# Kernel tuning notes

Measured on AMD Instinct MI355X. Metric: run time of the kernel, lower is better.

Reference implementation:

```python
import jax, jax.numpy as jnp
import numpy as np

NUM_NODES = 10000
NUM_EDGES = 640000
D_FEAT = 128

def setup_inputs() -> dict:
    key = jax.random.key(0)
    k1, k2 = jax.random.split(key)
    x = jax.random.normal(k1, (NUM_NODES, D_FEAT), dtype=jnp.float32)
    edge_index = jax.random.randint(k2, (2, NUM_EDGES), 0, NUM_NODES, dtype=jnp.int64)
    return {"x": x, "edge_index": edge_index}

def reference(x, edge_index):
    # MessagePassing(aggr='add') with default message/update:
    # msg = x[src]; out[n] = sum of msg over edges with dst == n
    src, dst = edge_index[0], edge_index[1]
    msg = x[src]                                   # [num_edges, d]
    out = jax.ops.segment_sum(msg, dst, num_segments=NUM_NODES)  # [num_nodes, d]
    return out
```

## Files before the change

kernel.cpp:

```cpp
#include <hip/hip_runtime.h>

#define NUM_NODES 10000
#define NUM_EDGES 640000
#define D_FEAT 128

#define NPB 20
#define NB 500
#define K1_BLOCKS 256
#define EPB (NUM_EDGES / K1_BLOCKS)
#define CELL_CAP 16
#define INV 0xFFFFFFFFu
#define ZROW 10000u
#define STRIPE 112
#define SCAP 108
#define MAXB (NPB * STRIPE)

#define XB_U4 (NUM_NODES * 16 + 16)
#define CVT_PER_BLOCK (NUM_NODES * 16 / K1_BLOCKS)

typedef __attribute__((ext_vector_type(2))) float f32x2;


__device__ __forceinline__ unsigned bf16_rne(float f) {
    unsigned u = __float_as_uint(f);
    return (u + 0x7FFFu + ((u >> 16) & 1u)) >> 16;
}

__device__ __forceinline__ int div20(int d) {
    return (int)(((unsigned)d * 104858u) >> 21);
}

__global__ __launch_bounds__(1024) void scatter_cvt_kernel(
    const int* __restrict__ ei, const float4* __restrict__ x4,
    uint4* __restrict__ xb, unsigned* __restrict__ ovfcell,
    uint4* __restrict__ slots4)
{
    __shared__ int cur[NB];
    __shared__ uint4 cellsv[NB * (CELL_CAP / 4)];
    __shared__ unsigned s_ovf[15];
    __shared__ int ovfcur;

    int t = threadIdx.x, b = blockIdx.x;
    if (t < NB) cur[t] = 0;
    if (t < 15) s_ovf[t] = 0;
    if (t == 0) ovfcur = 0;
    uint4 iv = make_uint4(INV, INV, INV, INV);
    if (t < 1000) { cellsv[t] = iv; cellsv[t + 1000] = iv; }

    int base = b * EPB;
    int s0 = ei[base + t];
    int d0 = ei[NUM_EDGES + base + t];
    int s1 = ei[base + t + 1024];
    int d1 = ei[NUM_EDGES + base + t + 1024];
    int s2 = 0, d2 = 0;
    bool has2 = (t + 2048) < EPB;
    if (has2) {
        s2 = ei[base + t + 2048];
        d2 = ei[NUM_EDGES + base + t + 2048];
    }

    if (t < CVT_PER_BLOCK) {
        int o = b * CVT_PER_BLOCK + t;
        float4 a = x4[2 * o];
        float4 c = x4[2 * o + 1];
        uint4 w;
        w.x = bf16_rne(a.x) | (bf16_rne(a.y) << 16);
        w.y = bf16_rne(a.z) | (bf16_rne(a.w) << 16);
        w.z = bf16_rne(c.x) | (bf16_rne(c.y) << 16);
        w.w = bf16_rne(c.z) | (bf16_rne(c.w) << 16);
        xb[o] = w;
    }
    if (b == 0 && t < 16)
        xb[NUM_NODES * 16 + t] = make_uint4(0u, 0u, 0u, 0u);
    __syncthreads();

    unsigned* cells = (unsigned*)cellsv;
    {
        int k = div20(d0), m = d0 - k * NPB;
        int pos = atomicAdd(&cur[k], 1);
        if (pos < CELL_CAP)
            cells[k * CELL_CAP + pos] = ((unsigned)m << 16) | (unsigned)s0;
        else {
            int o = atomicAdd(&ovfcur, 1);
            if (o < 15) s_ovf[o] = ((unsigned)k << 19) |
                                   ((unsigned)m << 14) | (unsigned)s0;
        }
    }
    {
        int k = div20(d1), m = d1 - k * NPB;
        int pos = atomicAdd(&cur[k], 1);
        if (pos < CELL_CAP)
            cells[k * CELL_CAP + pos] = ((unsigned)m << 16) | (unsigned)s1;
        else {
            int o = atomicAdd(&ovfcur, 1);
            if (o < 15) s_ovf[o] = ((unsigned)k << 19) |
                                   ((unsigned)m << 14) | (unsigned)s1;
        }
    }
    if (has2) {
        int k = div20(d2), m = d2 - k * NPB;
        int pos = atomicAdd(&cur[k], 1);
        if (pos < CELL_CAP)
            cells[k * CELL_CAP + pos] = ((unsigned)m << 16) | (unsigned)s2;
        else {
            int o = atomicAdd(&ovfcur, 1);
            if (o < 15) s_ovf[o] = ((unsigned)k << 19) |
                                   ((unsigned)m << 14) | (unsigned)s2;
        }
    }
    __syncthreads();

    for (int idx = t; idx < NB * (CELL_CAP / 4); idx += 1024)
        slots4[((unsigned)(idx >> 2) * K1_BLOCKS + (unsigned)b) *
               (CELL_CAP / 4) + (unsigned)(idx & 3)] = cellsv[idx];
    if (t < 15) ovfcell[b * 16 + t] = s_ovf[t];
    if (t == 15) ovfcell[b * 16 + 15] = (unsigned)min(ovfcur, 15);
}

__device__ __forceinline__ void acc8p(f32x2* a, uint4 w) {
    f32x2 v;
    v.x = __uint_as_float(w.x << 16);
    v.y = __uint_as_float(w.x & 0xFFFF0000u);
    a[0] += v;
    v.x = __uint_as_float(w.y << 16);
    v.y = __uint_as_float(w.y & 0xFFFF0000u);
    a[1] += v;
    v.x = __uint_as_float(w.z << 16);
    v.y = __uint_as_float(w.z & 0xFFFF0000u);
    a[2] += v;
    v.x = __uint_as_float(w.w << 16);
    v.y = __uint_as_float(w.w & 0xFFFF0000u);
    a[3] += v;
}

__global__ __launch_bounds__(640, 5) void sort_gather_kernel(
    const uint4* __restrict__ xb,
    const uint4* __restrict__ slots4,
    const unsigned* __restrict__ ovfcell,
    float4* __restrict__ out4)
{
    __shared__ unsigned s_src[MAXB];
    __shared__ int cur20[NPB];
    __shared__ int s_ovfany;

    int k = blockIdx.x;
    int t = threadIdx.x;

    if (t < NPB) cur20[t] = t * STRIPE;
    if (t == 0) s_ovfany = 0;
    for (int i = t; i < MAXB; i += 640) s_src[i] = ZROW;

    if (t < K1_BLOCKS) {
        unsigned oc = ovfcell[t * 16 + 15];
        if (oc) atomicOr(&s_ovfany, 1);
    }

    const uint4* sb = slots4 + (unsigned)k * 1024u;
    uint4 w40 = sb[t];
    uint4 w41 = (t < 384) ? sb[t + 640] : make_uint4(INV, INV, INV, INV);
    __syncthreads();

    {
        unsigned m;
        m = w40.x >> 16; if (m < NPB) { int p = atomicAdd(&cur20[m], 1); if (p < (int)(m * STRIPE + SCAP)) s_src[p] = w40.x & 0xFFFFu; }
        m = w40.y >> 16; if (m < NPB) { int p = atomicAdd(&cur20[m], 1); if (p < (int)(m * STRIPE + SCAP)) s_src[p] = w40.y & 0xFFFFu; }
        m = w40.z >> 16; if (m < NPB) { int p = atomicAdd(&cur20[m], 1); if (p < (int)(m * STRIPE + SCAP)) s_src[p] = w40.z & 0xFFFFu; }
        m = w40.w >> 16; if (m < NPB) { int p = atomicAdd(&cur20[m], 1); if (p < (int)(m * STRIPE + SCAP)) s_src[p] = w40.w & 0xFFFFu; }
        m = w41.x >> 16; if (m < NPB) { int p = atomicAdd(&cur20[m], 1); if (p < (int)(m * STRIPE + SCAP)) s_src[p] = w41.x & 0xFFFFu; }
        m = w41.y >> 16; if (m < NPB) { int p = atomicAdd(&cur20[m], 1); if (p < (int)(m * STRIPE + SCAP)) s_src[p] = w41.y & 0xFFFFu; }
        m = w41.z >> 16; if (m < NPB) { int p = atomicAdd(&cur20[m], 1); if (p < (int)(m * STRIPE + SCAP)) s_src[p] = w41.z & 0xFFFFu; }
        m = w41.w >> 16; if (m < NPB) { int p = atomicAdd(&cur20[m], 1); if (p < (int)(m * STRIPE + SCAP)) s_src[p] = w41.w & 0xFFFFu; }
    }
    if (s_ovfany && t < K1_BLOCKS) {
        int oc = (int)min(ovfcell[t * 16 + 15], 15u);
        for (int i = 0; i < oc; ++i) {
            unsigned e = ovfcell[t * 16 + i];
            if ((int)(e >> 19) == k) {
                unsigned m = (e >> 14) & 31u;
                int p = atomicAdd(&cur20[m], 1);
                if (p < (int)(m * STRIPE + SCAP)) s_src[p] = e & 0x3FFFu;
            }
        }
    }
    __syncthreads();

    int wave = t >> 6;
    int lane = t & 63;
    int q    = lane >> 4;
    int sub  = lane & 15;

    #pragma unroll
    for (int half = 0; half < 2; ++half) {
        int m = wave + half * 10;
        int ecRaw = cur20[m] - m * STRIPE;
        f32x2 a[4];
        a[0] = 0.f; a[1] = 0.f; a[2] = 0.f; a[3] = 0.f;

        if (ecRaw <= SCAP) {
            int bA = m * STRIPE;
            int eA = (ecRaw + 3) & ~3;
            unsigned s = s_src[bA + q];
            uint4 r = xb[s * 16u + (unsigned)sub];
            for (int j = 0; j < eA; j += 4) {
                unsigned s2 = s_src[bA + j + 4 + q];
                uint4 r2 = xb[s2 * 16u + (unsigned)sub];
                acc8p(a, r);
                r = r2;
            }
        } else {
            const unsigned* sw = (const unsigned*)sb;
            for (int idx = q; idx < K1_BLOCKS * CELL_CAP; idx += 4) {
                unsigned w = sw[idx];
                if ((w >> 16) == (unsigned)m) {
                    uint4 r = xb[(w & 0xFFFFu) * 16u + (unsigned)sub];
                    acc8p(a, r);
                }
            }
            if (s_ovfany && q == 0) {
                for (int bb = 0; bb < K1_BLOCKS; ++bb) {
                    int oc = (int)min(ovfcell[bb * 16 + 15], 15u);
                    for (int i = 0; i < oc; ++i) {
                        unsigned e = ovfcell[bb * 16 + i];
                        if ((int)(e >> 19) == k &&
                            (int)((e >> 14) & 31u) == m) {
                            uint4 r = xb[(e & 0x3FFFu) * 16u + (unsigned)sub];
                            acc8p(a, r);
                        }
                    }
                }
            }
        }

        #pragma unroll
        for (int r = 0; r < 4; ++r) {
            a[r].x += __shfl_down(a[r].x, 32);
            a[r].y += __shfl_down(a[r].y, 32);
            a[r].x += __shfl_down(a[r].x, 16);
            a[r].y += __shfl_down(a[r].y, 16);
        }
        if (q == 0) {
            unsigned o = (unsigned)(k * NPB + m) * 32u + (unsigned)sub * 2u;
            out4[o]     = make_float4(a[0].x, a[0].y, a[1].x, a[1].y);
            out4[o + 1] = make_float4(a[2].x, a[2].y, a[3].x, a[3].y);
        }
    }
}

extern "C" void kernel_launch(void* const* d_in, const int* in_sizes, int n_in,
                              void* d_out, int out_size, void* d_ws, size_t ws_size,
                              hipStream_t stream) {
    const float* x   = (const float*)d_in[0];
    const int*   ei  = (const int*)d_in[1];
    float*       out = (float*)d_out;

    uint4*    xb      = (uint4*)d_ws;
    unsigned* ovfcell = (unsigned*)(xb + XB_U4);
    uint4*    slots4  = (uint4*)(ovfcell + K1_BLOCKS * 16);

    scatter_cvt_kernel<<<K1_BLOCKS, 1024, 0, stream>>>(
        ei, (const float4*)x, xb, ovfcell, slots4);

    sort_gather_kernel<<<NB, 640, 0, stream>>>(
        xb, (const uint4*)slots4, ovfcell, (float4*)out);
}
```

Measured before the change: 80.96 us.

## Double scatter blocks, halve cell capacity, and store slots block-major

The scatter kernel now runs 512 blocks of 512 threads instead of 256 of 1024, with per-block cell capacity cut from 16 to 8. Each block writes its cells as one contiguous stream, so stores are coalesced, and the gather kernel reads them transposed with strided uint4 loads. The aim is more parallelism and cheaper coalesced writes in the first kernel, paid for by scattered reads in the second. Smaller cells could overflow more often, which would push more edges onto the slow overflow path.

Result: slower. 84.65 us (+4.6%).

```diff
diff --git a/kernel.cpp b/kernel.cpp
--- a/kernel.cpp
+++ b/kernel.cpp
@@ -6,9 +6,10 @@
 
 #define NPB 20
 #define NB 500
-#define K1_BLOCKS 256
-#define EPB (NUM_EDGES / K1_BLOCKS)
-#define CELL_CAP 16
+#define K1B 512
+#define K1T 512
+#define EPB (NUM_EDGES / K1B)
+#define CELL_CAP 8
 #define INV 0xFFFFFFFFu
 #define ZROW 10000u
 #define STRIPE 112
@@ -16,7 +17,7 @@
 #define MAXB (NPB * STRIPE)
 
 #define XB_U4 (NUM_NODES * 16 + 16)
-#define CVT_PER_BLOCK (NUM_NODES * 16 / K1_BLOCKS)
+#define CPB 313
 
 typedef __attribute__((ext_vector_type(2))) float f32x2;
 
@@ -30,7 +31,7 @@
     return (int)(((unsigned)d * 104858u) >> 21);
 }
 
-__global__ __launch_bounds__(1024) void scatter_cvt_kernel(
+__global__ __launch_bounds__(K1T, 4) void scatter_cvt_kernel(
     const int* __restrict__ ei, const float4* __restrict__ x4,
     uint4* __restrict__ xb, unsigned* __restrict__ ovfcell,
     uint4* __restrict__ slots4)
@@ -45,30 +46,33 @@
     if (t < 15) s_ovf[t] = 0;
     if (t == 0) ovfcur = 0;
     uint4 iv = make_uint4(INV, INV, INV, INV);
-    if (t < 1000) { cellsv[t] = iv; cellsv[t + 1000] = iv; }
+    cellsv[t] = iv;
+    if (t < 488) cellsv[t + 512] = iv;
 
     int base = b * EPB;
     int s0 = ei[base + t];
     int d0 = ei[NUM_EDGES + base + t];
-    int s1 = ei[base + t + 1024];
-    int d1 = ei[NUM_EDGES + base + t + 1024];
+    int s1 = ei[base + t + 512];
+    int d1 = ei[NUM_EDGES + base + t + 512];
     int s2 = 0, d2 = 0;
-    bool has2 = (t + 2048) < EPB;
+    bool has2 = t < (EPB - 1024);
     if (has2) {
-        s2 = ei[base + t + 2048];
-        d2 = ei[NUM_EDGES + base + t + 2048];
-    }
-
-    if (t < CVT_PER_BLOCK) {
-        int o = b * CVT_PER_BLOCK + t;
-        float4 a = x4[2 * o];
-        float4 c = x4[2 * o + 1];
-        uint4 w;
-        w.x = bf16_rne(a.x) | (bf16_rne(a.y) << 16);
-        w.y = bf16_rne(a.z) | (bf16_rne(a.w) << 16);
-        w.z = bf16_rne(c.x) | (bf16_rne(c.y) << 16);
-        w.w = bf16_rne(c.z) | (bf16_rne(c.w) << 16);
-        xb[o] = w;
+        s2 = ei[base + t + 1024];
+        d2 = ei[NUM_EDGES + base + t + 1024];
+    }
+
+    if (t < CPB) {
+        int o = b * CPB + t;
+        if (o < NUM_NODES * 16) {
+            float4 a = x4[2 * o];
+            float4 c = x4[2 * o + 1];
+            uint4 w;
+            w.x = bf16_rne(a.x) | (bf16_rne(a.y) << 16);
+            w.y = bf16_rne(a.z) | (bf16_rne(a.w) << 16);
+            w.z = bf16_rne(c.x) | (bf16_rne(c.y) << 16);
+            w.w = bf16_rne(c.z) | (bf16_rne(c.w) << 16);
+            xb[o] = w;
+        }
     }
     if (b == 0 && t < 16)
         xb[NUM_NODES * 16 + t] = make_uint4(0u, 0u, 0u, 0u);
@@ -110,9 +114,9 @@
     }
     __syncthreads();
 
-    for (int idx = t; idx < NB * (CELL_CAP / 4); idx += 1024)
-        slots4[((unsigned)(idx >> 2) * K1_BLOCKS + (unsigned)b) *
-               (CELL_CAP / 4) + (unsigned)(idx & 3)] = cellsv[idx];
+    slots4[(unsigned)b * 1000u + (unsigned)t] = cellsv[t];
+    if (t < 488)
+        slots4[(unsigned)b * 1000u + (unsigned)(t + 512)] = cellsv[t + 512];
     if (t < 15) ovfcell[b * 16 + t] = s_ovf[t];
     if (t == 15) ovfcell[b * 16 + 15] = (unsigned)min(ovfcur, 15);
 }
@@ -150,14 +154,23 @@
     if (t == 0) s_ovfany = 0;
     for (int i = t; i < MAXB; i += 640) s_src[i] = ZROW;
 
-    if (t < K1_BLOCKS) {
+    if (t < K1B) {
         unsigned oc = ovfcell[t * 16 + 15];
         if (oc) atomicOr(&s_ovfany, 1);
     }
 
-    const uint4* sb = slots4 + (unsigned)k * 1024u;
-    uint4 w40 = sb[t];
-    uint4 w41 = (t < 384) ? sb[t + 640] : make_uint4(INV, INV, INV, INV);
+    uint4 w40, w41 = make_uint4(INV, INV, INV, INV);
+    {
+        unsigned c1 = ((unsigned)(t >> 1) * (unsigned)NB + (unsigned)k) * 2u +
+                      (unsigned)(t & 1);
+        w40 = slots4[c1];
+    }
+    if (t < 384) {
+        int tt = t + 640;
+        unsigned c2 = ((unsigned)(tt >> 1) * (unsigned)NB + (unsigned)k) * 2u +
+                      (unsigned)(tt & 1);
+        w41 = slots4[c2];
+    }
     __syncthreads();
 
     {
@@ -171,7 +184,7 @@
         m = w41.z >> 16; if (m < NPB) { int p = atomicAdd(&cur20[m], 1); if (p < (int)(m * STRIPE + SCAP)) s_src[p] = w41.z & 0xFFFFu; }
         m = w41.w >> 16; if (m < NPB) { int p = atomicAdd(&cur20[m], 1); if (p < (int)(m * STRIPE + SCAP)) s_src[p] = w41.w & 0xFFFFu; }
     }
-    if (s_ovfany && t < K1_BLOCKS) {
+    if (s_ovfany && t < K1B) {
         int oc = (int)min(ovfcell[t * 16 + 15], 15u);
         for (int i = 0; i < oc; ++i) {
             unsigned e = ovfcell[t * 16 + i];
@@ -208,16 +221,18 @@
                 r = r2;
             }
         } else {
-            const unsigned* sw = (const unsigned*)sb;
-            for (int idx = q; idx < K1_BLOCKS * CELL_CAP; idx += 4) {
-                unsigned w = sw[idx];
-                if ((w >> 16) == (unsigned)m) {
-                    uint4 r = xb[(w & 0xFFFFu) * 16u + (unsigned)sub];
+            const unsigned* sw = (const unsigned*)slots4;
+            for (int idx = q; idx < K1B * CELL_CAP; idx += 4) {
+                int bb = idx >> 3, w = idx & 7;
+                unsigned word = sw[((unsigned)bb * (unsigned)NB +
+                                    (unsigned)k) * 8u + (unsigned)w];
+                if ((word >> 16) == (unsigned)m) {
+                    uint4 r = xb[(word & 0xFFFFu) * 16u + (unsigned)sub];
                     acc8p(a, r);
                 }
             }
             if (s_ovfany && q == 0) {
-                for (int bb = 0; bb < K1_BLOCKS; ++bb) {
+                for (int bb = 0; bb < K1B; ++bb) {
                     int oc = (int)min(ovfcell[bb * 16 + 15], 15u);
                     for (int i = 0; i < oc; ++i) {
                         unsigned e = ovfcell[bb * 16 + i];
@@ -255,9 +270,9 @@
 
     uint4*    xb      = (uint4*)d_ws;
     unsigned* ovfcell = (unsigned*)(xb + XB_U4);
-    uint4*    slots4  = (uint4*)(ovfcell + K1_BLOCKS * 16);
-
-    scatter_cvt_kernel<<<K1_BLOCKS, 1024, 0, stream>>>(
+    uint4*    slots4  = (uint4*)(ovfcell + K1B * 16);
+
+    scatter_cvt_kernel<<<K1B, K1T, 0, stream>>>(
         ei, (const float4*)x, xb, ovfcell, slots4);
 
     sort_gather_kernel<<<NB, 640, 0, stream>>>(
```
